# Performance work log

Hardware: AMD Instinct MI355X
Metric: run time of the kernel (lower is better)

## Reference

```python
import jax, jax.numpy as jnp
import numpy as np

TOP_K = 8
ALPHA = 0.1
EPS = 1e-20


def setup_inputs() -> dict:
    key = jax.random.key(0)
    k1, k2 = jax.random.split(key)
    B, S, D, E = 4, 8192, 1024, 64
    hidden_states = jax.random.normal(k1, (B, S, D), dtype=jnp.float32)
    # kaiming_uniform_(a=sqrt(5)) on [E, D] -> bound = 1/sqrt(D)
    bound = 1.0 / np.sqrt(D)
    W = jax.random.uniform(k2, (E, D), dtype=jnp.float32, minval=-bound, maxval=bound)
    return {"hidden_states": hidden_states, "W": W}


def reference(hidden_states, W):
    B, S, D = hidden_states.shape
    E = W.shape[0]
    x = hidden_states.reshape(-1, D)                       # [T, D], T = B*S
    logits = jnp.einsum('td,ed->te', x, W)                 # [T, E]
    scores = jax.nn.softmax(logits, axis=-1)               # [T, E]
    top_k_weights, top_k_idx = jax.lax.top_k(scores, TOP_K)  # [T, K]
    # norm_topk_experts renormalization
    top_k_weights = top_k_weights / (top_k_weights.sum(axis=-1, keepdims=True) + EPS)
    # seq_aux loss: per-batch expert selection counts via scatter-add
    idx = top_k_idx.reshape(B, -1)                         # [B, S*K]
    ce = jnp.zeros((B, E), dtype=jnp.float32).at[jnp.arange(B)[:, None], idx].add(1.0)
    mean_scores = scores.reshape(B, S, E).mean(axis=1)     # [B, E]
    aux_loss = (ce * mean_scores).sum(axis=1).mean() * ALPHA
    return top_k_idx, top_k_weights, aux_loss
```

## Files before the change

### kernel.cpp

```cpp
#include <hip/hip_runtime.h>
#include <hip/hip_bf16.h>

#define TOKS   32768
#define NEXP   64
#define DDIM   1024
#define SEQ    8192
#define NBATCH 4
#define TPB    64
#define STR    68
#define CSTR   21
#define BK     128
#define NCH    (DDIM / BK)
#define ASTR   136

typedef __attribute__((ext_vector_type(8))) short short8v;
typedef __attribute__((ext_vector_type(4))) float f32x4;

__device__ __forceinline__ void stage4(ushort* dh, ushort* dl, float4 v) {
  __hip_bfloat162 h0 = __float22bfloat162_rn(make_float2(v.x, v.y));
  __hip_bfloat162 h1 = __float22bfloat162_rn(make_float2(v.z, v.w));
  float2 f0 = __bfloat1622float2(h0);
  float2 f1 = __bfloat1622float2(h1);
  __hip_bfloat162 l0 = __float22bfloat162_rn(make_float2(v.x - f0.x, v.y - f0.y));
  __hip_bfloat162 l1 = __float22bfloat162_rn(make_float2(v.z - f1.x, v.w - f1.y));
  *(__hip_bfloat162*)(dh)     = h0;
  *(__hip_bfloat162*)(dh + 2) = h1;
  *(__hip_bfloat162*)(dl)     = l0;
  *(__hip_bfloat162*)(dl + 2) = l1;
}

__global__ __launch_bounds__(256, 2) void moe_gate_main(
    const float* __restrict__ X, const float* __restrict__ W,
    float* __restrict__ out, float* __restrict__ gsum, float* __restrict__ gce,
    int* __restrict__ flag_cnt, int* __restrict__ flag_tok)
{
  __shared__ __align__(16) char smem[4 * 64 * ASTR * 2];

  ushort* Ah = (ushort*)smem;
  ushort* Al = Ah + 64 * ASTR;
  ushort* Bh = Al + 64 * ASTR;
  ushort* Bl = Bh + 64 * ASTR;

  float* xs   = (float*)smem;
  float* wsm  = (float*)(smem + 17408);
  float* red  = (float*)(smem + 34816);
  float* gmx  = (float*)(smem + 35840);
  float* cval = (float*)(smem + 36096);
  int*   cidx = (int*)  (smem + 41472);
  int*   hist = (int*)  (smem + 46848);

  const int tid = threadIdx.x;
  const int tok_base = blockIdx.x * TPB;
  const int bb = blockIdx.x >> 7;

  const int l = tid & 63;
  const int q = tid >> 6;

  const int c4 = tid & 31;
  const int r0 = tid >> 5;

  const int wm = q >> 1, wn = q & 1;
  const int fr = l & 15;
  const int fk = (l >> 4) * 8;

  f32x4 accA[2][2], accB[2][2];
#pragma unroll
  for (int i = 0; i < 2; ++i)
#pragma unroll
    for (int j = 0; j < 2; ++j) {
      accA[i][j] = (f32x4)0.0f;
      accB[i][j] = (f32x4)0.0f;
    }

  float4 px[8], pw[8];
#pragma unroll
  for (int i = 0; i < 8; ++i) {
    px[i] = *(const float4*)(X + (size_t)(tok_base + r0 + 8 * i) * DDIM + 4 * c4);
    pw[i] = *(const float4*)(W + (size_t)(r0 + 8 * i) * DDIM + 4 * c4);
  }

#pragma unroll 1
  for (int kt = 0; kt < NCH; ++kt) {
    __syncthreads();
#pragma unroll
    for (int i = 0; i < 8; ++i) {
      const int row = r0 + 8 * i;
      stage4(&Ah[row * ASTR + 4 * c4], &Al[row * ASTR + 4 * c4], px[i]);
      stage4(&Bh[row * ASTR + 4 * c4], &Bl[row * ASTR + 4 * c4], pw[i]);
    }
    __syncthreads();
    if (kt + 1 < NCH) {
      const int db = (kt + 1) * BK;
#pragma unroll
      for (int i = 0; i < 8; ++i) {
        px[i] = *(const float4*)(X + (size_t)(tok_base + r0 + 8 * i) * DDIM + db + 4 * c4);
        pw[i] = *(const float4*)(W + (size_t)(r0 + 8 * i) * DDIM + db + 4 * c4);
      }
    }
#pragma unroll
    for (int s = 0; s < BK / 32; ++s) {
      const int ko = s * 32 + fk;
      short8v a_h[2], a_l[2], b_h[2], b_l[2];
#pragma unroll
      for (int i = 0; i < 2; ++i) {
        const ushort* pa = Ah + (size_t)(32 * wm + 16 * i + fr) * ASTR + ko;
        a_h[i] = *(const short8v*)pa;
        a_l[i] = *(const short8v*)(pa + 64 * ASTR);
        const ushort* pb = Bh + (size_t)(32 * wn + 16 * i + fr) * ASTR + ko;
        b_h[i] = *(const short8v*)pb;
        b_l[i] = *(const short8v*)(pb + 64 * ASTR);
      }
#pragma unroll
      for (int i = 0; i < 2; ++i)
#pragma unroll
        for (int j = 0; j < 2; ++j) {
          accA[i][j] = __builtin_amdgcn_mfma_f32_16x16x32_bf16(a_h[i], b_h[j], accA[i][j], 0, 0, 0);
          accB[i][j] = __builtin_amdgcn_mfma_f32_16x16x32_bf16(a_l[i], b_h[j], accB[i][j], 0, 0, 0);
          accA[i][j] = __builtin_amdgcn_mfma_f32_16x16x32_bf16(a_h[i], b_l[j], accA[i][j], 0, 0, 0);
        }
    }
  }

  __syncthreads();
#pragma unroll
  for (int i = 0; i < 2; ++i)
#pragma unroll
    for (int j = 0; j < 2; ++j) {
      f32x4 c = accA[i][j] + accB[i][j];
      const int tok = 32 * wm + 16 * i + 4 * (l >> 4);
      const int e   = 32 * wn + 16 * j + fr;
#pragma unroll
      for (int r = 0; r < 4; ++r)
        wsm[(tok + r) * STR + e] = c[r];
    }
  if (tid < 64) hist[tid] = 0;
  __syncthreads();

  float* logits  = wsm;
  float* scoresT = xs;
  const int t = l;

  float m = -__builtin_huge_valf();
#pragma unroll
  for (int e = 0; e < 16; ++e) m = fmaxf(m, logits[t * STR + q * 16 + e]);
  red[q * 64 + t] = m;
  __syncthreads();
  float gm = fmaxf(fmaxf(red[t], red[64 + t]), fmaxf(red[128 + t], red[192 + t]));
  if (q == 0) gmx[t] = gm;
  float z = 0.0f;
#pragma unroll
  for (int e = 0; e < 16; ++e) {
    float ev = expf(logits[t * STR + q * 16 + e] - gm);
    scoresT[(q * 16 + e) * STR + t] = ev;
    z += ev;
  }
  __syncthreads();
  red[q * 64 + t] = z;
  __syncthreads();
  float Z = red[t] + red[64 + t] + red[128 + t] + red[192 + t];
  float invZ = 1.0f / Z;
#pragma unroll
  for (int e = 0; e < 16; ++e) scoresT[(q * 16 + e) * STR + t] *= invZ;
  __syncthreads();

  {
    const int e = l, g = q;
    float s = 0.0f;
#pragma unroll
    for (int tt = 0; tt < 16; ++tt) s += scoresT[e * STR + g * 16 + tt];
    red[g * 64 + e] = s;
  }
  __syncthreads();
  if (tid < 64) {
    float tot = red[tid] + red[64 + tid] + red[128 + tid] + red[192 + tid];
    atomicAdd(&gsum[bb * 64 + tid], tot);
  }

  if (tid < 128) {
    const int h = tid >> 6;
    const int eb = h * 32;
#pragma unroll 1
    for (int k = 0; k < 9; ++k) {
      float mv = -1.0f; int mi = eb;
#pragma unroll 4
      for (int e = 0; e < 32; ++e) {
        float v = scoresT[(eb + e) * STR + t];
        if (v > mv) { mv = v; mi = eb + e; }
      }
      cval[t * CSTR + h * 9 + k] = mv;
      cidx[t * CSTR + h * 9 + k] = mi;
      scoresT[mi * STR + t] = -1.0f;
    }
  }
  __syncthreads();

  if (tid < 64) {
    float wv[9]; int wi[8];
#pragma unroll 1
    for (int k = 0; k < 9; ++k) {
      float mv = -1.0f; int mj = 0;
#pragma unroll 3
      for (int j = 0; j < 18; ++j) {
        float v = cval[t * CSTR + j];
        if (v > mv) { mv = v; mj = j; }
      }
      wv[k] = mv;
      if (k < 8) {
        wi[k] = cidx[t * CSTR + mj];
        atomicAdd(&hist[wi[k]], 1);
      }
      cval[t * CSTR + mj] = -1.0f;
    }
    bool flag = false;
#pragma unroll
    for (int k = 0; k < 8; ++k)
      if (wv[k + 1] >= wv[k] * (1.0f - 2.0e-5f)) flag = true;
    if (flag) {
      int p = atomicAdd(flag_cnt, 1);
      flag_tok[p] = tok_base + t;
    }
    double ed[8]; double den = 0.0;
#pragma unroll
    for (int k = 0; k < 8; ++k) {
      ed[k] = exp((double)logits[t * STR + wi[k]] - (double)gmx[t]);
      den += ed[k];
    }
    const size_t tg = (size_t)(tok_base + t);
    *(float4*)(out + tg * 8) =
        make_float4((float)wi[0], (float)wi[1], (float)wi[2], (float)wi[3]);
    *(float4*)(out + tg * 8 + 4) =
        make_float4((float)wi[4], (float)wi[5], (float)wi[6], (float)wi[7]);
    *(float4*)(out + (size_t)TOKS * 8 + tg * 8) =
        make_float4((float)(ed[0] / den), (float)(ed[1] / den),
                    (float)(ed[2] / den), (float)(ed[3] / den));
    *(float4*)(out + (size_t)TOKS * 8 + tg * 8 + 4) =
        make_float4((float)(ed[4] / den), (float)(ed[5] / den),
                    (float)(ed[6] / den), (float)(ed[7] / den));
  }
  __syncthreads();
  if (tid < 64) atomicAdd(&gce[bb * 64 + tid], (float)hist[tid]);
}

__global__ __launch_bounds__(256) void moe_refine(
    const float* __restrict__ X, const float* __restrict__ W,
    float* __restrict__ out, float* __restrict__ gce,
    const int* __restrict__ flag_cnt, const int* __restrict__ flag_tok)
{
  __shared__ __align__(16) float xrow[DDIM];
  __shared__ double part[4][NEXP];
  const int tid = threadIdx.x;
  const int n = *flag_cnt;
  const int e = tid & 63;
  const int c = tid >> 6;
#pragma unroll 1
  for (int it = blockIdx.x; it < n; it += 256) {
    const int tok = flag_tok[it];
    __syncthreads();
    *(float4*)&xrow[tid * 4] = *(const float4*)&X[(size_t)tok * DDIM + tid * 4];
    __syncthreads();
    const float* wr = W + (size_t)e * DDIM + c * 256;
    const float* xr = xrow + c * 256;
    double s0 = 0.0, s1 = 0.0, s2 = 0.0, s3 = 0.0;
#pragma unroll 4
    for (int j = 0; j < 256; j += 4) {
      s0 += (double)xr[j]     * (double)wr[j];
      s1 += (double)xr[j + 1] * (double)wr[j + 1];
      s2 += (double)xr[j + 2] * (double)wr[j + 2];
      s3 += (double)xr[j + 3] * (double)wr[j + 3];
    }
    part[c][e] = (s0 + s1) + (s2 + s3);
    __syncthreads();
    if (tid < 64) {
      double cur = (part[0][e] + part[1][e]) + (part[2][e] + part[3][e]);
      int wi[8]; double wl[8];
#pragma unroll 1
      for (int k = 0; k < 8; ++k) {
        double mv = cur; int mi = e;
#pragma unroll
        for (int off = 1; off < 64; off <<= 1) {
          double ov = __shfl_xor(mv, off);
          int    oi = __shfl_xor(mi, off);
          if (ov > mv || (ov == mv && oi < mi)) { mv = ov; mi = oi; }
        }
        wi[k] = mi; wl[k] = mv;
        if (e == mi) cur = -1.0e300;
      }
      if (e == 0) {
        int olde[8];
#pragma unroll
        for (int k = 0; k < 8; ++k) olde[k] = (int)out[(size_t)tok * 8 + k];
        double ex[8]; double den = 0.0;
#pragma unroll
        for (int k = 0; k < 8; ++k) { ex[k] = exp(wl[k] - wl[0]); den += ex[k]; }
#pragma unroll
        for (int k = 0; k < 8; ++k) {
          out[(size_t)tok * 8 + k] = (float)wi[k];
          out[(size_t)TOKS * 8 + (size_t)tok * 8 + k] = (float)(ex[k] / den);
        }
        const int bbb = tok >> 13;
#pragma unroll 1
        for (int k = 0; k < 8; ++k) {
          bool in_new = false, in_old = false;
          for (int j = 0; j < 8; ++j) {
            if (wi[j] == olde[k]) in_new = true;
            if (olde[j] == wi[k]) in_old = true;
          }
          if (!in_new) atomicAdd(&gce[bbb * 64 + olde[k]], -1.0f);
          if (!in_old) atomicAdd(&gce[bbb * 64 + wi[k]], 1.0f);
        }
      }
    }
  }
}

__global__ void moe_gate_aux(const float* __restrict__ gsum,
                             const float* __restrict__ gce,
                             float* __restrict__ out)
{
  __shared__ float r[256];
  const int tid = threadIdx.x;
  r[tid] = gce[tid] * gsum[tid];
  __syncthreads();
  for (int s = 128; s > 0; s >>= 1) {
    if (tid < s) r[tid] += r[tid + s];
    __syncthreads();
  }
  if (tid == 0)
    out[(size_t)TOKS * 16] = 0.1f * r[0] / ((float)SEQ * (float)NBATCH);
}

extern "C" void kernel_launch(void* const* d_in, const int* in_sizes, int n_in,
                              void* d_out, int out_size, void* d_ws, size_t ws_size,
                              hipStream_t stream)
{
  const float* X = (const float*)d_in[0];
  const float* W = (const float*)d_in[1];
  float* out  = (float*)d_out;
  float* gsum = (float*)d_ws;
  float* gce  = gsum + NBATCH * NEXP;
  int* flag_cnt = (int*)((char*)d_ws + 2048);
  int* flag_tok = (int*)((char*)d_ws + 2176);

  hipMemsetAsync(d_ws, 0, 2176, stream);
  moe_gate_main<<<TOKS / TPB, 256, 0, stream>>>(X, W, out, gsum, gce, flag_cnt, flag_tok);
  moe_refine<<<256, 256, 0, stream>>>(X, W, out, gce, flag_cnt, flag_tok);
  moe_gate_aux<<<1, 256, 0, stream>>>(gsum, gce, out);
}
```

Baseline: 228.1 us.

## Pre-split W into bf16 hi/lo once and stream it via direct-to-LDS loads

A new pre-kernel converts W into swizzled bf16 hi/lo tiles in workspace once per call, so the main kernel no longer converts W separately in every block. The main GEMM now keeps the X fragments in registers after converting them there, loads the W tiles straight into double-buffered shared memory with global_load_lds, and uses 32x32x16 MFMAs in place of 16x16x32. This removes the per-block W conversion and the X staging through shared memory, which cuts LDS traffic and barriers. The costs are an extra kernel launch plus a workspace buffer, and a hand-written bf16 rounding routine that must match the earlier split exactly.

```diff
diff --git a/kernel.cpp b/kernel.cpp
--- a/kernel.cpp
+++ b/kernel.cpp
@@ -1,5 +1,4 @@
 #include <hip/hip_runtime.h>
-#include <hip/hip_bf16.h>
 
 #define TOKS   32768
 #define NEXP   64
@@ -9,37 +8,69 @@
 #define TPB    64
 #define STR    68
 #define CSTR   21
-#define BK     128
-#define NCH    (DDIM / BK)
-#define ASTR   136
-
-typedef __attribute__((ext_vector_type(8))) short short8v;
-typedef __attribute__((ext_vector_type(4))) float f32x4;
-
-__device__ __forceinline__ void stage4(ushort* dh, ushort* dl, float4 v) {
-  __hip_bfloat162 h0 = __float22bfloat162_rn(make_float2(v.x, v.y));
-  __hip_bfloat162 h1 = __float22bfloat162_rn(make_float2(v.z, v.w));
-  float2 f0 = __bfloat1622float2(h0);
-  float2 f1 = __bfloat1622float2(h1);
-  __hip_bfloat162 l0 = __float22bfloat162_rn(make_float2(v.x - f0.x, v.y - f0.y));
-  __hip_bfloat162 l1 = __float22bfloat162_rn(make_float2(v.z - f1.x, v.w - f1.y));
-  *(__hip_bfloat162*)(dh)     = h0;
-  *(__hip_bfloat162*)(dh + 2) = h1;
-  *(__hip_bfloat162*)(dl)     = l0;
-  *(__hip_bfloat162*)(dl + 2) = l1;
+#define BK     64
+#define NCHK   (DDIM / BK)
+#define WTILE  (NEXP * 16 * 16)
+
+typedef __attribute__((ext_vector_type(8)))  short short8v;
+typedef __attribute__((ext_vector_type(16))) float f32x16;
+
+__device__ __forceinline__ unsigned f2bf(float x) {
+  unsigned u = __float_as_uint(x);
+  return (u + 0x7fffu + ((u >> 16) & 1u)) >> 16;
+}
+__device__ __forceinline__ float bf2f(unsigned h) { return __uint_as_float(h << 16); }
+
+__device__ __forceinline__ void gload_lds16(const void* g, void* s) {
+  __builtin_amdgcn_global_load_lds(
+      (const __attribute__((address_space(1))) unsigned int*)g,
+      (__attribute__((address_space(3))) unsigned int*)s, 16, 0, 0);
+}
+
+__device__ __forceinline__ void conv8(const float4 p0, const float4 p1,
+                                      unsigned* h, unsigned* lo) {
+  float ff[8] = {p0.x, p0.y, p0.z, p0.w, p1.x, p1.y, p1.z, p1.w};
+#pragma unroll
+  for (int i = 0; i < 4; ++i) {
+    unsigned h0 = f2bf(ff[2 * i]), h1 = f2bf(ff[2 * i + 1]);
+    h[i] = h0 | (h1 << 16);
+    unsigned l0 = f2bf(ff[2 * i] - bf2f(h0));
+    unsigned l1 = f2bf(ff[2 * i + 1] - bf2f(h1));
+    lo[i] = l0 | (l1 << 16);
+  }
+}
+
+__global__ void moe_wsplit(const float* __restrict__ W, ushort* __restrict__ W2) {
+  const int sid = blockIdx.x * 256 + threadIdx.x;
+  const int p  = sid & 15;
+  const int e  = (sid >> 4) & 63;
+  const int kc = sid >> 10;
+  const int sl = p ^ (e & 15);
+  const int k0 = kc * BK + (sl & 7) * 8;
+  const float* src = W + (size_t)e * DDIM + k0;
+  float f[8];
+  *(float4*)&f[0] = *(const float4*)src;
+  *(float4*)&f[4] = *(const float4*)(src + 4);
+  ushort o[8];
+  if (sl < 8) {
+#pragma unroll
+    for (int j = 0; j < 8; ++j) o[j] = (ushort)f2bf(f[j]);
+  } else {
+#pragma unroll
+    for (int j = 0; j < 8; ++j) {
+      unsigned hb = f2bf(f[j]);
+      o[j] = (ushort)f2bf(f[j] - bf2f(hb));
+    }
+  }
+  *(short8v*)(W2 + (size_t)sid * 8) = *(const short8v*)o;
 }
 
 __global__ __launch_bounds__(256, 2) void moe_gate_main(
-    const float* __restrict__ X, const float* __restrict__ W,
+    const float* __restrict__ X, const ushort* __restrict__ W2,
     float* __restrict__ out, float* __restrict__ gsum, float* __restrict__ gce,
     int* __restrict__ flag_cnt, int* __restrict__ flag_tok)
 {
-  __shared__ __align__(16) char smem[4 * 64 * ASTR * 2];
-
-  ushort* Ah = (ushort*)smem;
-  ushort* Al = Ah + 64 * ASTR;
-  ushort* Bh = Al + 64 * ASTR;
-  ushort* Bl = Bh + 64 * ASTR;
+  __shared__ __align__(16) char smem[47104];
 
   float* xs   = (float*)smem;
   float* wsm  = (float*)(smem + 17408);
@@ -53,86 +84,75 @@
   const int tok_base = blockIdx.x * TPB;
   const int bb = blockIdx.x >> 7;
 
-  const int l = tid & 63;
-  const int q = tid >> 6;
-
-  const int c4 = tid & 31;
-  const int r0 = tid >> 5;
-
+  const int l = tid & 63, q = tid >> 6;
   const int wm = q >> 1, wn = q & 1;
-  const int fr = l & 15;
-  const int fk = (l >> 4) * 8;
-
-  f32x4 accA[2][2], accB[2][2];
-#pragma unroll
-  for (int i = 0; i < 2; ++i)
-#pragma unroll
-    for (int j = 0; j < 2; ++j) {
-      accA[i][j] = (f32x4)0.0f;
-      accB[i][j] = (f32x4)0.0f;
-    }
-
-  float4 px[8], pw[8];
-#pragma unroll
-  for (int i = 0; i < 8; ++i) {
-    px[i] = *(const float4*)(X + (size_t)(tok_base + r0 + 8 * i) * DDIM + 4 * c4);
-    pw[i] = *(const float4*)(W + (size_t)(r0 + 8 * i) * DDIM + 4 * c4);
-  }
-
-#pragma unroll 1
-  for (int kt = 0; kt < NCH; ++kt) {
-    __syncthreads();
-#pragma unroll
-    for (int i = 0; i < 8; ++i) {
-      const int row = r0 + 8 * i;
-      stage4(&Ah[row * ASTR + 4 * c4], &Al[row * ASTR + 4 * c4], px[i]);
-      stage4(&Bh[row * ASTR + 4 * c4], &Bl[row * ASTR + 4 * c4], pw[i]);
-    }
-    __syncthreads();
-    if (kt + 1 < NCH) {
-      const int db = (kt + 1) * BK;
-#pragma unroll
-      for (int i = 0; i < 8; ++i) {
-        px[i] = *(const float4*)(X + (size_t)(tok_base + r0 + 8 * i) * DDIM + db + 4 * c4);
-        pw[i] = *(const float4*)(W + (size_t)(r0 + 8 * i) * DDIM + db + 4 * c4);
-      }
-    }
-#pragma unroll
-    for (int s = 0; s < BK / 32; ++s) {
-      const int ko = s * 32 + fk;
-      short8v a_h[2], a_l[2], b_h[2], b_l[2];
-#pragma unroll
-      for (int i = 0; i < 2; ++i) {
-        const ushort* pa = Ah + (size_t)(32 * wm + 16 * i + fr) * ASTR + ko;
-        a_h[i] = *(const short8v*)pa;
-        a_l[i] = *(const short8v*)(pa + 64 * ASTR);
-        const ushort* pb = Bh + (size_t)(32 * wn + 16 * i + fr) * ASTR + ko;
-        b_h[i] = *(const short8v*)pb;
-        b_l[i] = *(const short8v*)(pb + 64 * ASTR);
-      }
-#pragma unroll
-      for (int i = 0; i < 2; ++i)
-#pragma unroll
-        for (int j = 0; j < 2; ++j) {
-          accA[i][j] = __builtin_amdgcn_mfma_f32_16x16x32_bf16(a_h[i], b_h[j], accA[i][j], 0, 0, 0);
-          accB[i][j] = __builtin_amdgcn_mfma_f32_16x16x32_bf16(a_l[i], b_h[j], accB[i][j], 0, 0, 0);
-          accA[i][j] = __builtin_amdgcn_mfma_f32_16x16x32_bf16(a_h[i], b_l[j], accA[i][j], 0, 0, 0);
-        }
-    }
-  }
-
-  __syncthreads();
-#pragma unroll
-  for (int i = 0; i < 2; ++i)
-#pragma unroll
-    for (int j = 0; j < 2; ++j) {
-      f32x4 c = accA[i][j] + accB[i][j];
-      const int tok = 32 * wm + 16 * i + 4 * (l >> 4);
-      const int e   = 32 * wn + 16 * j + fr;
-#pragma unroll
-      for (int r = 0; r < 4; ++r)
-        wsm[(tok + r) * STR + e] = c[r];
-    }
+  const int rr = l & 31;
+  const int kh = l >> 5;
+
+  const float* xrow = X + (size_t)(tok_base + wm * 32 + rr) * DDIM + kh * 8;
+  const char* w2c = (const char*)W2;
+  const int btrow = (wn * 32 + rr) * 256;
+  const int bxor  = (wn * 32 + rr) & 15;
+
+  f32x16 acc = (f32x16)0.0f;
+  float4 px[8];
+  unsigned aH[16], aL[16];
+
+#pragma unroll
+  for (int s = 0; s < 4; ++s) {
+    px[2 * s]     = *(const float4*)(xrow + s * 16);
+    px[2 * s + 1] = *(const float4*)(xrow + s * 16 + 4);
+  }
+#pragma unroll
+  for (int i = 0; i < 4; ++i)
+    gload_lds16(w2c + q * 4096 + i * 1024 + l * 16, smem + q * 4096 + i * 1024);
+#pragma unroll
+  for (int s = 0; s < 4; ++s) conv8(px[2 * s], px[2 * s + 1], &aH[4 * s], &aL[4 * s]);
+  __syncthreads();
+
+  int cur = 0;
+#pragma unroll 1
+  for (int kc = 0; kc < NCHK; ++kc) {
+    if (kc + 1 < NCHK) {
+      const float* xr = xrow + (kc + 1) * BK;
+#pragma unroll
+      for (int s = 0; s < 4; ++s) {
+        px[2 * s]     = *(const float4*)(xr + s * 16);
+        px[2 * s + 1] = *(const float4*)(xr + s * 16 + 4);
+      }
+      const char* g = w2c + (size_t)(kc + 1) * WTILE + q * 4096 + l * 16;
+      char* d = smem + ((cur ^ 1) * 16384) + q * 4096;
+#pragma unroll
+      for (int i = 0; i < 4; ++i) gload_lds16(g + i * 1024, d + i * 1024);
+    }
+    const char* tb = smem + cur * 16384 + btrow;
+#pragma unroll
+    for (int s = 0; s < 4; ++s) {
+      short8v bh = *(const short8v*)(tb + (((2 * s + kh) ^ bxor) * 16));
+      short8v bl = *(const short8v*)(tb + (((8 + 2 * s + kh) ^ bxor) * 16));
+      union { short8v v; unsigned u[4]; } ua, ul;
+#pragma unroll
+      for (int i = 0; i < 4; ++i) { ua.u[i] = aH[4 * s + i]; ul.u[i] = aL[4 * s + i]; }
+      acc = __builtin_amdgcn_mfma_f32_32x32x16_bf16(ua.v, bh, acc, 0, 0, 0);
+      acc = __builtin_amdgcn_mfma_f32_32x32x16_bf16(ul.v, bh, acc, 0, 0, 0);
+      acc = __builtin_amdgcn_mfma_f32_32x32x16_bf16(ua.v, bl, acc, 0, 0, 0);
+    }
+    if (kc + 1 < NCHK) {
+#pragma unroll
+      for (int s = 0; s < 4; ++s) conv8(px[2 * s], px[2 * s + 1], &aH[4 * s], &aL[4 * s]);
+    }
+    __syncthreads();
+    cur ^= 1;
+  }
+
+  {
+    const int ccol = wn * 32 + rr;
+#pragma unroll
+    for (int r = 0; r < 16; ++r) {
+      const int trow = wm * 32 + (r & 3) + 8 * (r >> 2) + 4 * kh;
+      wsm[trow * STR + ccol] = acc[r];
+    }
+  }
   if (tid < 64) hist[tid] = 0;
   __syncthreads();
 
@@ -340,9 +360,11 @@
   float* gce  = gsum + NBATCH * NEXP;
   int* flag_cnt = (int*)((char*)d_ws + 2048);
   int* flag_tok = (int*)((char*)d_ws + 2176);
+  ushort* W2 = (ushort*)((char*)d_ws + (1 << 20));
 
   hipMemsetAsync(d_ws, 0, 2176, stream);
-  moe_gate_main<<<TOKS / TPB, 256, 0, stream>>>(X, W, out, gsum, gce, flag_cnt, flag_tok);
+  moe_wsplit<<<64, 256, 0, stream>>>(W, W2);
+  moe_gate_main<<<TOKS / TPB, 256, 0, stream>>>(X, W2, out, gsum, gce, flag_cnt, flag_tok);
   moe_refine<<<256, 256, 0, stream>>>(X, W, out, gce, flag_cnt, flag_tok);
   moe_gate_aux<<<1, 256, 0, stream>>>(gsum, gce, out);
 }
```

Measured after the change: 241.1 us. 1.06x slower.
